# Optimization experiments

Measured on AMD Instinct MI355X. Metric: run time of the kernel, lower is better.

Reference implementation:

```python
import jax, jax.numpy as jnp
import numpy as np

EPS = 1e-10
NUM_RELATION = 4
N_NODES = 50000
N_EDGES = 800000
D_IN = 128
D_H = 256


def rgc_layer(x, src, dst, rel, rel_w, rel_b, loop_w, loop_b):
    # torchdrug RelationalGraphConv: scatter-mean per (node, relation), then
    # linear over concatenated per-relation features + self-loop linear + relu.
    N, d = x.shape
    msg = x[src]                                      # [E, d] gather
    idx = dst * NUM_RELATION + rel                    # [E] bucket per (node, relation)
    num_seg = N * NUM_RELATION
    agg = jax.ops.segment_sum(msg, idx, num_segments=num_seg)            # [N*R, d]
    cnt = jax.ops.segment_sum(jnp.ones((msg.shape[0], 1), x.dtype), idx,
                              num_segments=num_seg)                       # [N*R, 1]
    update = (agg / (cnt + EPS)).reshape(N, NUM_RELATION * d)            # [N, R*d]
    out = update @ rel_w + rel_b + x @ loop_w + loop_b                   # [N, d_out]
    return jax.nn.relu(out)


def highway(x, hp_w, hp_b, ht_w, ht_b):
    proj = jax.nn.relu(x @ hp_w + hp_b)
    gate = jax.nn.sigmoid(x @ ht_w + ht_b)
    return gate * proj + (1.0 - gate) * x


def setup_inputs() -> dict:
    key = jax.random.key(0)
    ks = jax.random.split(key, 16)
    s = 0.02
    inp = {
        "x": jax.random.normal(ks[0], (N_NODES, D_IN), dtype=jnp.float32),
        "src": jax.random.randint(ks[1], (N_EDGES,), 0, N_NODES, dtype=jnp.int32),
        "dst": jax.random.randint(ks[2], (N_EDGES,), 0, N_NODES, dtype=jnp.int32),
        "rel": jax.random.randint(ks[3], (N_EDGES,), 0, NUM_RELATION, dtype=jnp.int32),
        # layer 1: RGC(128->256) + Highway(256)
        "rel_w1": jax.random.normal(ks[4], (NUM_RELATION * D_IN, D_H), dtype=jnp.float32) * s,
        "rel_b1": jnp.zeros((D_H,), jnp.float32),
        "loop_w1": jax.random.normal(ks[5], (D_IN, D_H), dtype=jnp.float32) * s,
        "loop_b1": jnp.zeros((D_H,), jnp.float32),
        "hp_w1": jax.random.normal(ks[6], (D_H, D_H), dtype=jnp.float32) * s,
        "hp_b1": jnp.zeros((D_H,), jnp.float32),
        "ht_w1": jax.random.normal(ks[7], (D_H, D_H), dtype=jnp.float32) * s,
        "ht_b1": jnp.full((D_H,), -2.0, jnp.float32),  # transform.bias.data.fill_(-2.0)
        # layer 2: RGC(256->256) + Highway(256)
        "rel_w2": jax.random.normal(ks[8], (NUM_RELATION * D_H, D_H), dtype=jnp.float32) * s,
        "rel_b2": jnp.zeros((D_H,), jnp.float32),
        "loop_w2": jax.random.normal(ks[9], (D_H, D_H), dtype=jnp.float32) * s,
        "loop_b2": jnp.zeros((D_H,), jnp.float32),
        "hp_w2": jax.random.normal(ks[10], (D_H, D_H), dtype=jnp.float32) * s,
        "hp_b2": jnp.zeros((D_H,), jnp.float32),
        "ht_w2": jax.random.normal(ks[11], (D_H, D_H), dtype=jnp.float32) * s,
        "ht_b2": jnp.full((D_H,), -2.0, jnp.float32),
    }
    return inp


def reference(x, src, dst, rel,
              rel_w1, rel_b1, loop_w1, loop_b1, hp_w1, hp_b1, ht_w1, ht_b1,
              rel_w2, rel_b2, loop_w2, loop_b2, hp_w2, hp_b2, ht_w2, ht_b2):
    h = rgc_layer(x, src, dst, rel, rel_w1, rel_b1, loop_w1, loop_b1)
    h = highway(h, hp_w1, hp_b1, ht_w1, ht_b1)
    h = rgc_layer(h, src, dst, rel, rel_w2, rel_b2, loop_w2, loop_b2)
    h = highway(h, hp_w2, hp_b2, ht_w2, ht_b2)
    return h  # node_feature, shape [N, 256]
```

## Files before the change

### kernel.cpp

```cpp
#include <hip/hip_runtime.h>

typedef __bf16 bf16_t;
typedef __bf16 bf16x8 __attribute__((ext_vector_type(8)));
typedef __bf16 bf16x4 __attribute__((ext_vector_type(4)));
typedef float f32x4 __attribute__((ext_vector_type(4)));
typedef int i32x4 __attribute__((ext_vector_type(4)));

#define BM 128
#define BK 64

__device__ __forceinline__ void gload_lds16(const void* g, void* s) {
    __builtin_amdgcn_global_load_lds(
        (const __attribute__((address_space(1))) unsigned int*)g,
        (__attribute__((address_space(3))) unsigned int*)s, 16, 0, 0);
}

__global__ __launch_bounds__(256, 2) void gemm_k(
    const bf16_t* __restrict__ A, int lda, int M,
    const bf16_t* __restrict__ Bt, int K,
    const float* __restrict__ bias, int relu_flag,
    bf16_t* __restrict__ outb, int ldo, int ocol,
    int NTM)
{
    __shared__ __align__(16) bf16_t As[BM * BK];
    __shared__ __align__(16) bf16_t Bs[256 * BK];

    const int L   = blockIdx.x;
    const int xcd = L & 7;
    const int sup = L >> 3;
    const int mt  = sup * 8 + xcd;
    if (mt >= NTM) return;
    const int m0 = mt * BM;

    const int tid  = threadIdx.x;
    const int wave = tid >> 6, lane = tid & 63;
    const int wr   = wave >> 1, wc = wave & 1;
    const int lm   = lane & 15, quad = lane >> 4;

    const bf16_t* ag[4];
    const bf16_t* bg[8];
    #pragma unroll
    for (int j = 0; j < 4; j++) {
        int c   = j * 256 + tid;
        int row = c >> 3;
        int col = ((c & 7) ^ (row & 7)) << 3;
        int gm  = m0 + row; if (gm >= M) gm = M - 1;
        ag[j] = A + (size_t)gm * lda + col;
    }
    #pragma unroll
    for (int j = 0; j < 8; j++) {
        int c   = j * 256 + tid;
        int row = c >> 3;
        int col = ((c & 7) ^ (row & 7)) << 3;
        bg[j] = Bt + (size_t)row * K + col;
    }

    f32x4 acc[4][8] = {};

    for (int k0 = 0; k0 < K; k0 += BK) {
        __syncthreads();
        #pragma unroll
        for (int j = 0; j < 4; j++)
            gload_lds16(ag[j] + k0, As + (size_t)(j * 256 + tid) * 8);
        #pragma unroll
        for (int j = 0; j < 8; j++)
            gload_lds16(bg[j] + k0, Bs + (size_t)(j * 256 + tid) * 8);
        __syncthreads();

        #pragma unroll
        for (int h = 0; h < 2; h++) {
            bf16x8 af[4];
            #pragma unroll
            for (int i = 0; i < 4; i++) {
                int r = wr * 64 + i * 16 + lm;
                af[i] = *(const bf16x8*)&As[(size_t)(r * 8 + ((h * 4 + quad) ^ (r & 7))) * 8];
            }
            #pragma unroll
            for (int ni = 0; ni < 8; ni++) {
                int r = wc * 128 + ni * 16 + lm;
                bf16x8 bfr = *(const bf16x8*)&Bs[(size_t)(r * 8 + ((h * 4 + quad) ^ (r & 7))) * 8];
                #pragma unroll
                for (int mi = 0; mi < 4; mi++)
                    acc[mi][ni] = __builtin_amdgcn_mfma_f32_16x16x32_bf16(
                        af[mi], bfr, acc[mi][ni], 0, 0, 0);
            }
        }
    }

    #pragma unroll
    for (int mi = 0; mi < 4; mi++) {
        #pragma unroll
        for (int ni = 0; ni < 8; ni++) {
            int col = wc * 128 + ni * 16 + lm;
            float b = bias[col];
            #pragma unroll
            for (int r = 0; r < 4; r++) {
                int row = m0 + wr * 64 + mi * 16 + quad * 4 + r;
                if (row < M) {
                    float v = acc[mi][ni][r] + b;
                    if (relu_flag) v = fmaxf(v, 0.f);
                    outb[(size_t)row * ldo + ocol + col] = (bf16_t)v;
                }
            }
        }
    }
}

__global__ __launch_bounds__(256, 2) void gemm_hw2(
    const bf16_t* __restrict__ A, int M,
    const bf16_t* __restrict__ Bt,
    const float* __restrict__ bias,
    bf16_t* __restrict__ outb, int ldo, int ocol,
    float* __restrict__ outf, int NTM)
{
    __shared__ __align__(16) bf16_t As[128 * 64];
    __shared__ __align__(16) bf16_t Bs[256 * 64];

    const int L    = blockIdx.x;
    const int xcd  = L & 7;
    const int rest = L >> 3;
    const int nt   = rest & 1;
    const int sup  = rest >> 1;
    const int mt   = sup * 8 + xcd;
    if (mt >= NTM) return;
    const int m0 = mt * 128;

    const int tid  = threadIdx.x;
    const int wave = tid >> 6, lane = tid & 63;
    const int lm   = lane & 15, quad = lane >> 4;

    const bf16_t* ag[4];
    const bf16_t* bg[8];
    #pragma unroll
    for (int j = 0; j < 4; j++) {
        int c   = j * 256 + tid;
        int row = c >> 3;
        int col = ((c & 7) ^ (row & 7)) << 3;
        int gm  = m0 + row; if (gm >= M) gm = M - 1;
        ag[j] = A + (size_t)gm * 256 + col;
    }
    #pragma unroll
    for (int j = 0; j < 8; j++) {
        int c    = j * 256 + tid;
        int row  = c >> 3;
        int col  = ((c & 7) ^ (row & 7)) << 3;
        int grow = nt * 128 + row + ((row >= 128) ? 128 : 0);
        bg[j] = Bt + (size_t)grow * 256 + col;
    }

    f32x4 acc[2][16] = {};

    for (int k0 = 0; k0 < 256; k0 += 64) {
        __syncthreads();
        #pragma unroll
        for (int j = 0; j < 4; j++)
            gload_lds16(ag[j] + k0, As + (size_t)(j * 256 + tid) * 8);
        #pragma unroll
        for (int j = 0; j < 8; j++)
            gload_lds16(bg[j] + k0, Bs + (size_t)(j * 256 + tid) * 8);
        __syncthreads();

        #pragma unroll
        for (int h = 0; h < 2; h++) {
            bf16x8 af[2];
            #pragma unroll
            for (int i = 0; i < 2; i++) {
                int r = wave * 32 + i * 16 + lm;
                af[i] = *(const bf16x8*)&As[(size_t)(r * 8 + ((h * 4 + quad) ^ (r & 7))) * 8];
            }
            #pragma unroll
            for (int ni = 0; ni < 16; ni++) {
                int r = ni * 16 + lm;
                bf16x8 bfr = *(const bf16x8*)&Bs[(size_t)(r * 8 + ((h * 4 + quad) ^ (r & 7))) * 8];
                #pragma unroll
                for (int mi = 0; mi < 2; mi++)
                    acc[mi][ni] = __builtin_amdgcn_mfma_f32_16x16x32_bf16(
                        af[mi], bfr, acc[mi][ni], 0, 0, 0);
            }
        }
    }

    #pragma unroll
    for (int mi = 0; mi < 2; mi++) {
        #pragma unroll
        for (int ni = 0; ni < 8; ni++) {
            int col = nt * 128 + ni * 16 + lm;
            float bp  = bias[col];
            float bg2 = bias[256 + col];
            #pragma unroll
            for (int r = 0; r < 4; r++) {
                int row = m0 + wave * 32 + mi * 16 + quad * 4 + r;
                if (row < M) {
                    float p = acc[mi][ni][r] + bp;
                    float g = acc[mi][ni + 8][r] + bg2;
                    float s = 1.0f / (1.0f + __expf(-g));
                    float hv = (float)A[(size_t)row * 256 + col];
                    float v = s * fmaxf(p, 0.f) + (1.0f - s) * hv;
                    if (outf) outf[(size_t)row * 256 + col] = v;
                    else      outb[(size_t)row * ldo + ocol + col] = (bf16_t)v;
                }
            }
        }
    }
}

__global__ void prep_all(
    const float* __restrict__ rel_w1, const float* __restrict__ loop_w1,
    const float* __restrict__ rel_w2, const float* __restrict__ loop_w2,
    const float* __restrict__ hp_w1,  const float* __restrict__ ht_w1,
    const float* __restrict__ hp_w2,  const float* __restrict__ ht_w2,
    bf16_t* __restrict__ W1t, bf16_t* __restrict__ W2t,
    bf16_t* __restrict__ Wh1t, bf16_t* __restrict__ Wh2t,
    const float* __restrict__ rb1, const float* __restrict__ lb1,
    const float* __restrict__ rb2, const float* __restrict__ lb2,
    const float* __restrict__ hpb1, const float* __restrict__ htb1,
    const float* __restrict__ hpb2, const float* __restrict__ htb2,
    float* __restrict__ bR1, float* __restrict__ bR2,
    float* __restrict__ bH1, float* __restrict__ bH2,
    const float* __restrict__ x, bf16_t* __restrict__ A1, int N,
    int* __restrict__ cnt, int NSEG, int cvb)
{
    int b = blockIdx.x, tid = threadIdx.x;
    if (b < 2944) {
        const float* W; bf16_t* Wt; int ldk, k0, n0, base;
        if      (b < 512)  { W = rel_w1;  Wt = W1t;  ldk = 640;  k0 = 0;    n0 = 0;   base = 0; }
        else if (b < 640)  { W = loop_w1; Wt = W1t;  ldk = 640;  k0 = 512;  n0 = 0;   base = 512; }
        else if (b < 1664) { W = rel_w2;  Wt = W2t;  ldk = 1280; k0 = 0;    n0 = 0;   base = 640; }
        else if (b < 1920) { W = loop_w2; Wt = W2t;  ldk = 1280; k0 = 1024; n0 = 0;   base = 1664; }
        else if (b < 2176) { W = hp_w1;   Wt = Wh1t; ldk = 256;  k0 = 0;    n0 = 0;   base = 1920; }
        else if (b < 2432) { W = ht_w1;   Wt = Wh1t; ldk = 256;  k0 = 0;    n0 = 256; base = 2176; }
        else if (b < 2688) { W = hp_w2;   Wt = Wh2t; ldk = 256;  k0 = 0;    n0 = 0;   base = 2432; }
        else               { W = ht_w2;   Wt = Wh2t; ldk = 256;  k0 = 0;    n0 = 256; base = 2688; }
        int k = b - base;
        int n = tid;
        Wt[(size_t)(n0 + n) * ldk + k0 + k] = (bf16_t)W[(size_t)k * 256 + n];
    } else if (b == 2944) {
        int t = tid;
        bR1[t] = rb1[t] + lb1[t];
        bR2[t] = rb2[t] + lb2[t];
        bH1[t] = hpb1[t]; bH1[256 + t] = htb1[t];
        bH2[t] = hpb2[t]; bH2[256 + t] = htb2[t];
    } else if (b < 2945 + cvb) {
        int t = (b - 2945) * 256 + tid;
        if (t < N * 32) {
            int row = t >> 5, c = (t & 31) << 2;
            f32x4 v = *(const f32x4*)(x + (size_t)row * 128 + c);
            bf16x4 o;
            o[0] = (bf16_t)v[0]; o[1] = (bf16_t)v[1]; o[2] = (bf16_t)v[2]; o[3] = (bf16_t)v[3];
            *(bf16x4*)(A1 + (size_t)row * 640 + 512 + c) = o;
        }
    } else {
        int t = ((b - 2945 - cvb) * 256 + tid) * 4;
        if (t < NSEG) {
            i32x4 z = {0, 0, 0, 0};
            *(i32x4*)(cnt + t) = z;
        }
    }
}

__global__ void count_k(const int* __restrict__ dst, const int* __restrict__ rel,
                        int* __restrict__ cnt, int E)
{
    int e = blockIdx.x * blockDim.x + threadIdx.x;
    if (e < E) atomicAdd(&cnt[dst[e] * 4 + rel[e]], 1);
}

__global__ void scan_partial(const int* __restrict__ cnt, int* __restrict__ offs,
                             int* __restrict__ chunkSums, int NSEG)
{
    __shared__ int sh[256];
    int t = threadIdx.x;
    int idx = blockIdx.x * 256 + t;
    int v = (idx < NSEG) ? cnt[idx] : 0;
    sh[t] = v;
    __syncthreads();
    for (int d = 1; d < 256; d <<= 1) {
        int add = (t >= d) ? sh[t - d] : 0;
        __syncthreads();
        sh[t] += add;
        __syncthreads();
    }
    if (idx < NSEG) offs[idx] = sh[t] - v;
    if (t == 255) chunkSums[blockIdx.x] = sh[t];
}

__global__ void scan_chunks(int* __restrict__ chunkSums, int NCHUNK)
{
    __shared__ int sh[1024];
    int t = threadIdx.x;
    int v = (t < NCHUNK) ? chunkSums[t] : 0;
    sh[t] = v;
    __syncthreads();
    for (int d = 1; d < 1024; d <<= 1) {
        int add = (t >= d) ? sh[t - d] : 0;
        __syncthreads();
        sh[t] += add;
        __syncthreads();
    }
    if (t < NCHUNK) chunkSums[t] = sh[t] - v;
}

__global__ void scan_add(int* __restrict__ offs, const int* __restrict__ chunkSums,
                         int* __restrict__ cursor, int NSEG)
{
    int idx = blockIdx.x * 256 + threadIdx.x;
    if (idx < NSEG) {
        int o = offs[idx] + chunkSums[blockIdx.x];
        offs[idx] = o;
        cursor[idx] = o;
    }
}

__global__ void fill_k(const int* __restrict__ src, const int* __restrict__ dst,
                       const int* __restrict__ rel,
                       int* __restrict__ cursor, int* __restrict__ eidx, int E)
{
    int e = blockIdx.x * blockDim.x + threadIdx.x;
    if (e < E) {
        int seg = dst[e] * 4 + rel[e];
        int pos = atomicAdd(&cursor[seg], 1);
        eidx[pos] = src[e];
    }
}

__global__ void seg_mean256(const int* __restrict__ offs, const int* __restrict__ cnt,
                            const int* __restrict__ eidx,
                            const bf16_t* __restrict__ xb, int ldx,
                            bf16_t* __restrict__ Aout, int lda, int NSEG)
{
    int wv = (blockIdx.x << 2) + (threadIdx.x >> 6);
    if (wv >= NSEG) return;
    int lane = threadIdx.x & 63;
    int half = lane >> 5;
    int c = (lane & 31) << 3;
    int start = offs[wv];
    int n = cnt[wv];
    float acc[8] = {};
    int i = 0;
    for (; i + 8 <= n; i += 8) {
        int s0 = eidx[start + i + 0 + half];
        int s1 = eidx[start + i + 2 + half];
        int s2 = eidx[start + i + 4 + half];
        int s3 = eidx[start + i + 6 + half];
        bf16x8 v0 = *(const bf16x8*)(xb + (size_t)s0 * ldx + c);
        bf16x8 v1 = *(const bf16x8*)(xb + (size_t)s1 * ldx + c);
        bf16x8 v2 = *(const bf16x8*)(xb + (size_t)s2 * ldx + c);
        bf16x8 v3 = *(const bf16x8*)(xb + (size_t)s3 * ldx + c);
        #pragma unroll
        for (int j = 0; j < 8; j++)
            acc[j] += ((float)v0[j] + (float)v1[j]) + ((float)v2[j] + (float)v3[j]);
    }
    for (; i + 2 <= n; i += 2) {
        int s = eidx[start + i + half];
        bf16x8 v = *(const bf16x8*)(xb + (size_t)s * ldx + c);
        #pragma unroll
        for (int j = 0; j < 8; j++) acc[j] += (float)v[j];
    }
    if (i < n && half == 0) {
        int s = eidx[start + i];
        bf16x8 v = *(const bf16x8*)(xb + (size_t)s * ldx + c);
        #pragma unroll
        for (int j = 0; j < 8; j++) acc[j] += (float)v[j];
    }
    #pragma unroll
    for (int j = 0; j < 8; j++) acc[j] += __shfl_xor(acc[j], 32, 64);
    if (half == 0) {
        float inv = 1.0f / ((float)n + 1e-10f);
        int node = wv >> 2, r = wv & 3;
        bf16x8 o;
        #pragma unroll
        for (int j = 0; j < 8; j++) o[j] = (bf16_t)(acc[j] * inv);
        *(bf16x8*)(Aout + (size_t)node * lda + r * 256 + c) = o;
    }
}

__global__ void seg_mean128(const int* __restrict__ offs, const int* __restrict__ cnt,
                            const int* __restrict__ eidx,
                            const bf16_t* __restrict__ xb, int ldx,
                            bf16_t* __restrict__ Aout, int lda, int NSEG)
{
    int wv = (blockIdx.x << 2) + (threadIdx.x >> 6);
    if (wv >= NSEG) return;
    int lane = threadIdx.x & 63;
    int q = lane >> 4;
    int c = (lane & 15) << 3;
    int start = offs[wv];
    int n = cnt[wv];
    float acc[8] = {};
    int i = 0;
    for (; i + 8 <= n; i += 8) {
        int s0 = eidx[start + i + q];
        int s1 = eidx[start + i + 4 + q];
        bf16x8 v0 = *(const bf16x8*)(xb + (size_t)s0 * ldx + c);
        bf16x8 v1 = *(const bf16x8*)(xb + (size_t)s1 * ldx + c);
        #pragma unroll
        for (int j = 0; j < 8; j++) acc[j] += (float)v0[j] + (float)v1[j];
    }
    for (; i + 4 <= n; i += 4) {
        int s = eidx[start + i + q];
        bf16x8 v = *(const bf16x8*)(xb + (size_t)s * ldx + c);
        #pragma unroll
        for (int j = 0; j < 8; j++) acc[j] += (float)v[j];
    }
    if (q < n - i) {
        int s = eidx[start + i + q];
        bf16x8 v = *(const bf16x8*)(xb + (size_t)s * ldx + c);
        #pragma unroll
        for (int j = 0; j < 8; j++) acc[j] += (float)v[j];
    }
    #pragma unroll
    for (int j = 0; j < 8; j++) {
        acc[j] += __shfl_xor(acc[j], 16, 64);
        acc[j] += __shfl_xor(acc[j], 32, 64);
    }
    if (lane < 16) {
        float inv = 1.0f / ((float)n + 1e-10f);
        int node = wv >> 2, r = wv & 3;
        bf16x8 o;
        #pragma unroll
        for (int j = 0; j < 8; j++) o[j] = (bf16_t)(acc[j] * inv);
        *(bf16x8*)(Aout + (size_t)node * lda + r * 128 + c) = o;
    }
}

extern "C" void kernel_launch(void* const* d_in, const int* in_sizes, int n_in,
                              void* d_out, int out_size, void* d_ws, size_t ws_size,
                              hipStream_t stream)
{
    const float* x       = (const float*)d_in[0];
    const int*   src     = (const int*)d_in[1];
    const int*   dst     = (const int*)d_in[2];
    const int*   rel     = (const int*)d_in[3];
    const float* rel_w1  = (const float*)d_in[4];
    const float* rel_b1  = (const float*)d_in[5];
    const float* loop_w1 = (const float*)d_in[6];
    const float* loop_b1 = (const float*)d_in[7];
    const float* hp_w1   = (const float*)d_in[8];
    const float* hp_b1   = (const float*)d_in[9];
    const float* ht_w1   = (const float*)d_in[10];
    const float* ht_b1   = (const float*)d_in[11];
    const float* rel_w2  = (const float*)d_in[12];
    const float* rel_b2  = (const float*)d_in[13];
    const float* loop_w2 = (const float*)d_in[14];
    const float* loop_b2 = (const float*)d_in[15];
    const float* hp_w2   = (const float*)d_in[16];
    const float* hp_b2   = (const float*)d_in[17];
    const float* ht_w2   = (const float*)d_in[18];
    const float* ht_b2   = (const float*)d_in[19];

    const int N = in_sizes[0] / 128;
    const int E = in_sizes[1];
    const int NSEG = N * 4;
    const int NCHUNK = (NSEG + 255) / 256;
    float* out = (float*)d_out;

    char* ws = (char*)d_ws;
    size_t off = 0;
    auto alloc = [&](size_t bytes) {
        void* p = ws + off;
        off += (bytes + 255) & ~(size_t)255;
        return p;
    };
    int*    cnt    = (int*)alloc((size_t)NSEG * 4);
    int*    offs   = (int*)alloc((size_t)NSEG * 4);
    int*    cursor = (int*)alloc((size_t)NSEG * 4);
    int*    chunkS = (int*)alloc(4096);
    int*    eidx   = (int*)alloc((size_t)E * 4);
    bf16_t* A1     = (bf16_t*)alloc((size_t)N * 640 * 2);
    bf16_t* A2     = (bf16_t*)alloc((size_t)N * 1280 * 2);
    bf16_t* h      = (bf16_t*)alloc((size_t)N * 256 * 2);
    bf16_t* W1t    = (bf16_t*)alloc((size_t)256 * 640 * 2);
    bf16_t* W2t    = (bf16_t*)alloc((size_t)256 * 1280 * 2);
    bf16_t* Wh1t   = (bf16_t*)alloc((size_t)512 * 256 * 2);
    bf16_t* Wh2t   = (bf16_t*)alloc((size_t)512 * 256 * 2);
    float*  bR1    = (float*)alloc(256 * 4);
    float*  bR2    = (float*)alloc(256 * 4);
    float*  bH1    = (float*)alloc(512 * 4);
    float*  bH2    = (float*)alloc(512 * 4);

    dim3 blk(256);
    const int NTM = (N + BM - 1) / BM;
    const int supers = (NTM + 7) / 8;
    const int gridRGC = supers * 8;
    const int gridHW  = supers * 8 * 2;

    const int cvb = (N * 32 + 255) / 256;
    const int zb  = (NSEG / 4 + 255) / 256;
    prep_all<<<dim3(2945 + cvb + zb), blk, 0, stream>>>(
        rel_w1, loop_w1, rel_w2, loop_w2, hp_w1, ht_w1, hp_w2, ht_w2,
        W1t, W2t, Wh1t, Wh2t,
        rel_b1, loop_b1, rel_b2, loop_b2, hp_b1, ht_b1, hp_b2, ht_b2,
        bR1, bR2, bH1, bH2,
        x, A1, N, cnt, NSEG, cvb);

    count_k<<<dim3((E + 255) / 256), blk, 0, stream>>>(dst, rel, cnt, E);
    scan_partial<<<dim3(NCHUNK), blk, 0, stream>>>(cnt, offs, chunkS, NSEG);
    scan_chunks<<<dim3(1), dim3(1024), 0, stream>>>(chunkS, NCHUNK);
    scan_add<<<dim3(NCHUNK), blk, 0, stream>>>(offs, chunkS, cursor, NSEG);
    fill_k<<<dim3((E + 255) / 256), blk, 0, stream>>>(src, dst, rel, cursor, eidx, E);

    seg_mean128<<<dim3((NSEG + 3) / 4), blk, 0, stream>>>(offs, cnt, eidx,
                                                          A1 + 512, 640, A1, 640, NSEG);
    gemm_k<<<dim3(gridRGC), blk, 0, stream>>>(A1, 640, N, W1t, 640,
                                              bR1, 1, h, 256, 0, NTM);
    gemm_hw2<<<dim3(gridHW), blk, 0, stream>>>(h, N, Wh1t, bH1,
                                               A2, 1280, 1024, nullptr, NTM);

    seg_mean256<<<dim3((NSEG + 3) / 4), blk, 0, stream>>>(offs, cnt, eidx,
                                                          A2 + 1024, 1280, A2, 1280, NSEG);
    gemm_k<<<dim3(gridRGC), blk, 0, stream>>>(A2, 1280, N, W2t, 1280,
                                              bR2, 1, h, 256, 0, NTM);
    gemm_hw2<<<dim3(gridHW), blk, 0, stream>>>(h, N, Wh2t, bH2,
                                               nullptr, 0, 0, out, NTM);
}
```

Before: 513.8 us.

## Tile weight transpose via LDS, vectorize edge kernels, rework 256-wide segment mean

The weight transpose in prep_all now stages 16 rows in shared memory per block, so each thread writes 16 contiguous bf16 values instead of issuing one scattered 2-byte store. The count and fill edge kernels each handle four edges per thread using vector index loads. seg_mean256 switches from two half-waves to four quarter-waves, each covering the full 256-wide row with 16 accumulators, so more edges are in flight at once. Segment-mean outputs are written with nontemporal stores. The extra accumulators raise register pressure, and per-thread atomics become more serialized.

```diff
diff --git a/kernel.cpp b/kernel.cpp
--- a/kernel.cpp
+++ b/kernel.cpp
@@ -220,28 +220,40 @@
     const float* __restrict__ x, bf16_t* __restrict__ A1, int N,
     int* __restrict__ cnt, int NSEG, int cvb)
 {
+    __shared__ float sh[16][256];
     int b = blockIdx.x, tid = threadIdx.x;
-    if (b < 2944) {
-        const float* W; bf16_t* Wt; int ldk, k0, n0, base;
-        if      (b < 512)  { W = rel_w1;  Wt = W1t;  ldk = 640;  k0 = 0;    n0 = 0;   base = 0; }
-        else if (b < 640)  { W = loop_w1; Wt = W1t;  ldk = 640;  k0 = 512;  n0 = 0;   base = 512; }
-        else if (b < 1664) { W = rel_w2;  Wt = W2t;  ldk = 1280; k0 = 0;    n0 = 0;   base = 640; }
-        else if (b < 1920) { W = loop_w2; Wt = W2t;  ldk = 1280; k0 = 1024; n0 = 0;   base = 1664; }
-        else if (b < 2176) { W = hp_w1;   Wt = Wh1t; ldk = 256;  k0 = 0;    n0 = 0;   base = 1920; }
-        else if (b < 2432) { W = ht_w1;   Wt = Wh1t; ldk = 256;  k0 = 0;    n0 = 256; base = 2176; }
-        else if (b < 2688) { W = hp_w2;   Wt = Wh2t; ldk = 256;  k0 = 0;    n0 = 0;   base = 2432; }
-        else               { W = ht_w2;   Wt = Wh2t; ldk = 256;  k0 = 0;    n0 = 256; base = 2688; }
-        int k = b - base;
-        int n = tid;
-        Wt[(size_t)(n0 + n) * ldk + k0 + k] = (bf16_t)W[(size_t)k * 256 + n];
-    } else if (b == 2944) {
+    if (b < 184) {
+        const float* W; bf16_t* Wt; int ldk, k0, n0, kb;
+        if      (b < 32)  { W = rel_w1;  Wt = W1t;  ldk = 640;  k0 = 0;    n0 = 0;   kb = b; }
+        else if (b < 40)  { W = loop_w1; Wt = W1t;  ldk = 640;  k0 = 512;  n0 = 0;   kb = b - 32; }
+        else if (b < 104) { W = rel_w2;  Wt = W2t;  ldk = 1280; k0 = 0;    n0 = 0;   kb = b - 40; }
+        else if (b < 120) { W = loop_w2; Wt = W2t;  ldk = 1280; k0 = 1024; n0 = 0;   kb = b - 104; }
+        else if (b < 136) { W = hp_w1;   Wt = Wh1t; ldk = 256;  k0 = 0;    n0 = 0;   kb = b - 120; }
+        else if (b < 152) { W = ht_w1;   Wt = Wh1t; ldk = 256;  k0 = 0;    n0 = 256; kb = b - 136; }
+        else if (b < 168) { W = hp_w2;   Wt = Wh2t; ldk = 256;  k0 = 0;    n0 = 0;   kb = b - 152; }
+        else              { W = ht_w2;   Wt = Wh2t; ldk = 256;  k0 = 0;    n0 = 256; kb = b - 168; }
+        int kb16 = kb * 16;
+        #pragma unroll
+        for (int kk = 0; kk < 16; kk++)
+            sh[kk][tid] = W[(size_t)(kb16 + kk) * 256 + tid];
+        __syncthreads();
+        bf16x8 o0, o1;
+        #pragma unroll
+        for (int j = 0; j < 8; j++) {
+            o0[j] = (bf16_t)sh[j][tid];
+            o1[j] = (bf16_t)sh[8 + j][tid];
+        }
+        bf16_t* p = Wt + (size_t)(n0 + tid) * ldk + k0 + kb16;
+        *(bf16x8*)p = o0;
+        *(bf16x8*)(p + 8) = o1;
+    } else if (b == 184) {
         int t = tid;
         bR1[t] = rb1[t] + lb1[t];
         bR2[t] = rb2[t] + lb2[t];
         bH1[t] = hpb1[t]; bH1[256 + t] = htb1[t];
         bH2[t] = hpb2[t]; bH2[256 + t] = htb2[t];
-    } else if (b < 2945 + cvb) {
-        int t = (b - 2945) * 256 + tid;
+    } else if (b < 185 + cvb) {
+        int t = (b - 185) * 256 + tid;
         if (t < N * 32) {
             int row = t >> 5, c = (t & 31) << 2;
             f32x4 v = *(const f32x4*)(x + (size_t)row * 128 + c);
@@ -250,7 +262,7 @@
             *(bf16x4*)(A1 + (size_t)row * 640 + 512 + c) = o;
         }
     } else {
-        int t = ((b - 2945 - cvb) * 256 + tid) * 4;
+        int t = ((b - 185 - cvb) * 256 + tid) * 4;
         if (t < NSEG) {
             i32x4 z = {0, 0, 0, 0};
             *(i32x4*)(cnt + t) = z;
@@ -261,8 +273,17 @@
 __global__ void count_k(const int* __restrict__ dst, const int* __restrict__ rel,
                         int* __restrict__ cnt, int E)
 {
-    int e = blockIdx.x * blockDim.x + threadIdx.x;
-    if (e < E) atomicAdd(&cnt[dst[e] * 4 + rel[e]], 1);
+    int e = (blockIdx.x * blockDim.x + threadIdx.x) * 4;
+    if (e + 4 <= E) {
+        i32x4 d = *(const i32x4*)(dst + e);
+        i32x4 r = *(const i32x4*)(rel + e);
+        atomicAdd(&cnt[d[0] * 4 + r[0]], 1);
+        atomicAdd(&cnt[d[1] * 4 + r[1]], 1);
+        atomicAdd(&cnt[d[2] * 4 + r[2]], 1);
+        atomicAdd(&cnt[d[3] * 4 + r[3]], 1);
+    } else {
+        for (int k = e; k < E; k++) atomicAdd(&cnt[dst[k] * 4 + rel[k]], 1);
+    }
 }
 
 __global__ void scan_partial(const int* __restrict__ cnt, int* __restrict__ offs,
@@ -315,11 +336,21 @@
                        const int* __restrict__ rel,
                        int* __restrict__ cursor, int* __restrict__ eidx, int E)
 {
-    int e = blockIdx.x * blockDim.x + threadIdx.x;
-    if (e < E) {
-        int seg = dst[e] * 4 + rel[e];
-        int pos = atomicAdd(&cursor[seg], 1);
-        eidx[pos] = src[e];
+    int e = (blockIdx.x * blockDim.x + threadIdx.x) * 4;
+    if (e + 4 <= E) {
+        i32x4 s = *(const i32x4*)(src + e);
+        i32x4 d = *(const i32x4*)(dst + e);
+        i32x4 r = *(const i32x4*)(rel + e);
+        #pragma unroll
+        for (int k = 0; k < 4; k++) {
+            int pos = atomicAdd(&cursor[d[k] * 4 + r[k]], 1);
+            eidx[pos] = s[k];
+        }
+    } else {
+        for (int k = e; k < E; k++) {
+            int pos = atomicAdd(&cursor[dst[k] * 4 + rel[k]], 1);
+            eidx[pos] = src[k];
+        }
     }
 }
 
@@ -331,46 +362,66 @@
     int wv = (blockIdx.x << 2) + (threadIdx.x >> 6);
     if (wv >= NSEG) return;
     int lane = threadIdx.x & 63;
-    int half = lane >> 5;
-    int c = (lane & 31) << 3;
+    int q = lane >> 4;
+    int c = (lane & 15) << 3;
     int start = offs[wv];
     int n = cnt[wv];
-    float acc[8] = {};
+    float acc[16] = {};
     int i = 0;
     for (; i + 8 <= n; i += 8) {
-        int s0 = eidx[start + i + 0 + half];
-        int s1 = eidx[start + i + 2 + half];
-        int s2 = eidx[start + i + 4 + half];
-        int s3 = eidx[start + i + 6 + half];
-        bf16x8 v0 = *(const bf16x8*)(xb + (size_t)s0 * ldx + c);
-        bf16x8 v1 = *(const bf16x8*)(xb + (size_t)s1 * ldx + c);
-        bf16x8 v2 = *(const bf16x8*)(xb + (size_t)s2 * ldx + c);
-        bf16x8 v3 = *(const bf16x8*)(xb + (size_t)s3 * ldx + c);
-        #pragma unroll
-        for (int j = 0; j < 8; j++)
-            acc[j] += ((float)v0[j] + (float)v1[j]) + ((float)v2[j] + (float)v3[j]);
-    }
-    for (; i + 2 <= n; i += 2) {
-        int s = eidx[start + i + half];
-        bf16x8 v = *(const bf16x8*)(xb + (size_t)s * ldx + c);
-        #pragma unroll
-        for (int j = 0; j < 8; j++) acc[j] += (float)v[j];
-    }
-    if (i < n && half == 0) {
-        int s = eidx[start + i];
-        bf16x8 v = *(const bf16x8*)(xb + (size_t)s * ldx + c);
-        #pragma unroll
-        for (int j = 0; j < 8; j++) acc[j] += (float)v[j];
-    }
-    #pragma unroll
-    for (int j = 0; j < 8; j++) acc[j] += __shfl_xor(acc[j], 32, 64);
-    if (half == 0) {
+        int s0 = eidx[start + i + q];
+        int s1 = eidx[start + i + 4 + q];
+        const bf16_t* p0 = xb + (size_t)s0 * ldx + c;
+        const bf16_t* p1 = xb + (size_t)s1 * ldx + c;
+        bf16x8 a0 = *(const bf16x8*)p0;
+        bf16x8 a1 = *(const bf16x8*)(p0 + 128);
+        bf16x8 b0 = *(const bf16x8*)p1;
+        bf16x8 b1 = *(const bf16x8*)(p1 + 128);
+        #pragma unroll
+        for (int j = 0; j < 8; j++) {
+            acc[j]     += (float)a0[j] + (float)b0[j];
+            acc[j + 8] += (float)a1[j] + (float)b1[j];
+        }
+    }
+    for (; i + 4 <= n; i += 4) {
+        int s = eidx[start + i + q];
+        const bf16_t* p = xb + (size_t)s * ldx + c;
+        bf16x8 a0 = *(const bf16x8*)p;
+        bf16x8 a1 = *(const bf16x8*)(p + 128);
+        #pragma unroll
+        for (int j = 0; j < 8; j++) {
+            acc[j]     += (float)a0[j];
+            acc[j + 8] += (float)a1[j];
+        }
+    }
+    if (q < n - i) {
+        int s = eidx[start + i + q];
+        const bf16_t* p = xb + (size_t)s * ldx + c;
+        bf16x8 a0 = *(const bf16x8*)p;
+        bf16x8 a1 = *(const bf16x8*)(p + 128);
+        #pragma unroll
+        for (int j = 0; j < 8; j++) {
+            acc[j]     += (float)a0[j];
+            acc[j + 8] += (float)a1[j];
+        }
+    }
+    #pragma unroll
+    for (int j = 0; j < 16; j++) {
+        acc[j] += __shfl_xor(acc[j], 16, 64);
+        acc[j] += __shfl_xor(acc[j], 32, 64);
+    }
+    if (lane < 16) {
         float inv = 1.0f / ((float)n + 1e-10f);
         int node = wv >> 2, r = wv & 3;
-        bf16x8 o;
-        #pragma unroll
-        for (int j = 0; j < 8; j++) o[j] = (bf16_t)(acc[j] * inv);
-        *(bf16x8*)(Aout + (size_t)node * lda + r * 256 + c) = o;
+        bf16x8 o0, o1;
+        #pragma unroll
+        for (int j = 0; j < 8; j++) {
+            o0[j] = (bf16_t)(acc[j] * inv);
+            o1[j] = (bf16_t)(acc[j + 8] * inv);
+        }
+        bf16_t* dstp = Aout + (size_t)node * lda + r * 256 + c;
+        __builtin_nontemporal_store(o0, (bf16x8*)dstp);
+        __builtin_nontemporal_store(o1, (bf16x8*)(dstp + 128));
     }
 }
 
@@ -419,7 +470,7 @@
         bf16x8 o;
         #pragma unroll
         for (int j = 0; j < 8; j++) o[j] = (bf16_t)(acc[j] * inv);
-        *(bf16x8*)(Aout + (size_t)node * lda + r * 128 + c) = o;
+        __builtin_nontemporal_store(o, (bf16x8*)(Aout + (size_t)node * lda + r * 128 + c));
     }
 }
 
@@ -486,18 +537,19 @@
 
     const int cvb = (N * 32 + 255) / 256;
     const int zb  = (NSEG / 4 + 255) / 256;
-    prep_all<<<dim3(2945 + cvb + zb), blk, 0, stream>>>(
+    prep_all<<<dim3(185 + cvb + zb), blk, 0, stream>>>(
         rel_w1, loop_w1, rel_w2, loop_w2, hp_w1, ht_w1, hp_w2, ht_w2,
         W1t, W2t, Wh1t, Wh2t,
         rel_b1, loop_b1, rel_b2, loop_b2, hp_b1, ht_b1, hp_b2, ht_b2,
         bR1, bR2, bH1, bH2,
         x, A1, N, cnt, NSEG, cvb);
 
-    count_k<<<dim3((E + 255) / 256), blk, 0, stream>>>(dst, rel, cnt, E);
+    const int e4b = ((E + 3) / 4 + 255) / 256;
+    count_k<<<dim3(e4b), blk, 0, stream>>>(dst, rel, cnt, E);
     scan_partial<<<dim3(NCHUNK), blk, 0, stream>>>(cnt, offs, chunkS, NSEG);
     scan_chunks<<<dim3(1), dim3(1024), 0, stream>>>(chunkS, NCHUNK);
     scan_add<<<dim3(NCHUNK), blk, 0, stream>>>(offs, chunkS, cursor, NSEG);
-    fill_k<<<dim3((E + 255) / 256), blk, 0, stream>>>(src, dst, rel, cursor, eidx, E);
+    fill_k<<<dim3(e4b), blk, 0, stream>>>(src, dst, rel, cursor, eidx, E);
 
     seg_mean128<<<dim3((NSEG + 3) / 4), blk, 0, stream>>>(offs, cnt, eidx,
                                                           A1 + 512, 640, A1, 640, NSEG);
```

After: 528.4 us. 2.8% more time.
